# Performance work log

Hardware: AMD Instinct MI355X
Metric: run time of the kernel (lower is better)

## Reference

```python
import jax, jax.numpy as jnp
import numpy as np

B, N, D, H = 2, 1536, 1024, 16
DH = D // H
SCALE = DH ** -0.5


def setup_inputs() -> dict:
    key = jax.random.key(0)
    ks = jax.random.split(key, 16)
    s = D ** -0.5
    x = jax.random.normal(ks[0], (B, N, D), dtype=jnp.float32)
    # causal prior: 0 on/below diagonal, -1e9 above
    causal = jnp.tril(jnp.ones((N, N), dtype=bool))
    attn_bias = jnp.where(causal, 0.0, -1e9).astype(jnp.float32)[None, None]
    mk = lambda k, shp: jax.random.normal(k, shp, dtype=jnp.float32) * s
    return {
        "x": x,
        "attn_bias": attn_bias,
        "Wq": mk(ks[1], (D, D)), "bq": jnp.zeros((D,), jnp.float32),
        "Wk": mk(ks[2], (D, D)), "bk": jnp.zeros((D,), jnp.float32),
        "Wv": mk(ks[3], (D, D)), "bv": jnp.zeros((D,), jnp.float32),
        "Wg1": mk(ks[4], (D, D)), "bg1": jnp.zeros((D,), jnp.float32),
        "Wg2": mk(ks[5], (D, 1)), "bg2": jnp.zeros((1,), jnp.float32),
        "Wo": mk(ks[6], (D, D)), "bo": jnp.zeros((D,), jnp.float32),
    }


def reference(x, attn_bias, Wq, bq, Wk, bk, Wv, bv, Wg1, bg1, Wg2, bg2, Wo, bo):
    b, n, d = x.shape
    # projections -> [B, H, N, DH]
    split = lambda t: t.reshape(b, n, H, DH).swapaxes(1, 2)
    Q = split(x @ Wq + bq)
    K = split(x @ Wk + bk)
    V = split(x @ Wv + bv)
    # scores [B, H, N, N]
    attn = jnp.einsum("bhnd,bhmd->bhnm", Q, K) * SCALE + attn_bias
    attn = jax.nn.softmax(attn, axis=-1)
    # per-(batch, head, query) entropy over key axis
    entropy = -(attn * jnp.log(attn + 1e-6)).sum(-1)  # [B, H, N]
    # gate MLP (torch nn.GELU default is exact erf)
    gate = jax.nn.sigmoid(jax.nn.gelu(x @ Wg1 + bg1, approximate=False) @ Wg2 + bg2)  # [B, N, 1]
    attn = attn * gate[:, None, :, :]  # broadcast over heads, keys
    out = jnp.einsum("bhnm,bhmd->bhnd", attn, V)
    out = out.swapaxes(1, 2).reshape(b, n, d) @ Wo + bo
    return out, entropy
```

## Files before the change

kernel.cpp:

```cpp
#include <hip/hip_runtime.h>
#include <hip/hip_bf16.h>
#include <math.h>

#define Bsz  2
#define Nseq 1536
#define Dmod 1024
#define NH   16
#define DHd  64
#define MTOT (Bsz*Nseq)
#define SCALE 0.125f
#define BK   32

typedef short  short8 __attribute__((ext_vector_type(8)));
typedef float  f32x4  __attribute__((ext_vector_type(4)));
typedef unsigned short u16x4 __attribute__((ext_vector_type(4)));
typedef unsigned short ushortT;

__device__ __forceinline__ float b2f(__hip_bfloat16 v) { return __bfloat162float(v); }
__device__ __forceinline__ unsigned short f2bf(float f) {
    union { float f; unsigned u; } a; a.f = f;
    unsigned r = a.u + 0x7fffu + ((a.u >> 16) & 1u);
    return (unsigned short)(r >> 16);
}

__device__ __forceinline__ void gl2lds16(const ushortT* g, ushortT* lds) {
    __builtin_amdgcn_global_load_lds(
        (const __attribute__((address_space(1))) unsigned int*)(g),
        (__attribute__((address_space(3))) unsigned int*)(lds),
        16, 0, 0);
}

__global__ __launch_bounds__(256)
void prep_kernel(const float* W0, const float* W1, const float* W2,
                 const float* W3, const float* W4,
                 ushortT* T0, ushortT* T1, ushortT* T2, ushortT* T3, ushortT* T4,
                 const float* __restrict__ x, ushortT* __restrict__ xb,
                 float* __restrict__ glogit)
{
    const int z = blockIdx.z;
    const int t = threadIdx.x;
    if (z == 5) {
        const int bi = blockIdx.y * 16 + blockIdx.x;
        const size_t NEl = (size_t)MTOT * Dmod;
        for (size_t i = ((size_t)bi * 256 + t) * 4; i < NEl; i += (size_t)256 * 256 * 4) {
            float4 v = *(const float4*)(x + i);
            u16x4 o = { f2bf(v.x), f2bf(v.y), f2bf(v.z), f2bf(v.w) };
            *(u16x4*)(xb + i) = o;
        }
        if (t < 12) glogit[bi * 12 + t] = 0.f;
        return;
    }
    __shared__ float tile[64][65];
    const float* W = z == 0 ? W0 : z == 1 ? W1 : z == 2 ? W2 : z == 3 ? W3 : W4;
    ushortT*     T = z == 0 ? T0 : z == 1 ? T1 : z == 2 ? T2 : z == 3 ? T3 : T4;
    const int k0 = blockIdx.x * 64, n0 = blockIdx.y * 64;
    for (int i = t; i < 1024; i += 256) {
        int r = i >> 4, c4 = (i & 15) * 4;
        float4 v = *(const float4*)&W[(size_t)(k0 + r) * 1024 + n0 + c4];
        tile[r][c4 + 0] = v.x; tile[r][c4 + 1] = v.y;
        tile[r][c4 + 2] = v.z; tile[r][c4 + 3] = v.w;
    }
    __syncthreads();
    for (int i = t; i < 1024; i += 256) {
        int rn = i >> 4, ck4 = (i & 15) * 4;
        u16x4 o = { f2bf(tile[ck4 + 0][rn]), f2bf(tile[ck4 + 1][rn]),
                    f2bf(tile[ck4 + 2][rn]), f2bf(tile[ck4 + 3][rn]) };
        *(u16x4*)&T[(size_t)(n0 + rn) * 1024 + k0 + ck4] = o;
    }
}

__device__ __forceinline__
void gemm_core(const ushortT* __restrict__ A, const ushortT* __restrict__ Bt,
               int m0, int n0, ushortT* As, ushortT* Bs, f32x4 (&acc)[4][2])
{
    const int t = threadIdx.x;
    const int l = t & 63, w = t >> 6;
    const int wm = (w >> 1) * 64, wn = (w & 1) * 32;
    const int lm = l & 15, q = l >> 4;

    const int r0 = t >> 2, c0 = (t & 3) * 8;
    const ushortT* Ag0 = A  + (size_t)(m0 + r0) * 1024 + c0;
    const ushortT* Ag1 = Ag0 + (size_t)64 * 1024;
    const ushortT* Bg0 = Bt + (size_t)(n0 + r0) * 1024 + c0;
    ushortT* La0 = As + t * 8;
    ushortT* La1 = As + 2048 + t * 8;
    ushortT* Lb0 = Bs + t * 8;

    gl2lds16(Ag0, La0);
    gl2lds16(Ag1, La1);
    gl2lds16(Bg0, Lb0);

    for (int kt = 0; kt < 1024 / BK; ++kt) {
        __syncthreads();
        if (kt + 1 < 1024 / BK) {
            int ko = (kt + 1) * BK;
            int bo = ((kt + 1) & 1) ? 4096 : 0;
            int bo2 = ((kt + 1) & 1) ? 2048 : 0;
            gl2lds16(Ag0 + ko, La0 + bo);
            gl2lds16(Ag1 + ko, La1 + bo);
            gl2lds16(Bg0 + ko, Lb0 + bo2);
        }
        const ushortT* Ab = As + ((kt & 1) ? 4096 : 0);
        const ushortT* Bb = Bs + ((kt & 1) ? 2048 : 0);
        short8 af[4], bf[2];
#pragma unroll
        for (int i = 0; i < 4; ++i)
            af[i] = *(const short8*)&Ab[(wm + i * 16 + lm) * 32 + q * 8];
#pragma unroll
        for (int j = 0; j < 2; ++j)
            bf[j] = *(const short8*)&Bb[(wn + j * 16 + lm) * 32 + q * 8];
#pragma unroll
        for (int i = 0; i < 4; ++i)
#pragma unroll
            for (int j = 0; j < 2; ++j)
                acc[i][j] = __builtin_amdgcn_mfma_f32_16x16x32_bf16(af[i], bf[j], acc[i][j], 0, 0, 0);
    }
}

__device__ __forceinline__
void gemm_core_sq(const ushortT* __restrict__ A, const ushortT* __restrict__ Bt,
                  int m0, int n0, ushortT* As, ushortT* Bs, f32x4 (&acc)[2][2])
{
    const int t = threadIdx.x;
    const int l = t & 63, w = t >> 6;
    const int wm = (w >> 1) * 32, wn = (w & 1) * 32;
    const int lm = l & 15, q = l >> 4;

    const int r0 = t >> 2, c0 = (t & 3) * 8;
    const ushortT* Ag = A  + (size_t)(m0 + r0) * 1024 + c0;
    const ushortT* Bg = Bt + (size_t)(n0 + r0) * 1024 + c0;
    ushortT* La = As + t * 8;
    ushortT* Lb = Bs + t * 8;

    gl2lds16(Ag, La);
    gl2lds16(Bg, Lb);

    for (int kt = 0; kt < 1024 / BK; ++kt) {
        __syncthreads();
        if (kt + 1 < 1024 / BK) {
            int ko = (kt + 1) * BK;
            int bo = ((kt + 1) & 1) ? 2048 : 0;
            gl2lds16(Ag + ko, La + bo);
            gl2lds16(Bg + ko, Lb + bo);
        }
        const ushortT* Ab = As + ((kt & 1) ? 2048 : 0);
        const ushortT* Bb = Bs + ((kt & 1) ? 2048 : 0);
        short8 af[2], bf[2];
#pragma unroll
        for (int i = 0; i < 2; ++i) {
            af[i] = *(const short8*)&Ab[(wm + i * 16 + lm) * 32 + q * 8];
            bf[i] = *(const short8*)&Bb[(wn + i * 16 + lm) * 32 + q * 8];
        }
#pragma unroll
        for (int i = 0; i < 2; ++i)
#pragma unroll
            for (int j = 0; j < 2; ++j)
                acc[i][j] = __builtin_amdgcn_mfma_f32_16x16x32_bf16(af[i], bf[j], acc[i][j], 0, 0, 0);
    }
}

__global__ __launch_bounds__(256)
void gemm_qkvg(const ushortT* __restrict__ xb,
               const ushortT* Wt0, const ushortT* Wt1, const ushortT* Wt2, const ushortT* Wt3,
               const float* bz0, const float* bz1, const float* bz2, const float* bz3,
               const float* __restrict__ Wg2,
               ushortT* O0, ushortT* O1, ushortT* O2, float* __restrict__ glogit)
{
    __shared__ ushortT As[2 * 128 * 32];
    __shared__ ushortT Bs[2 * 64 * 32];
    const int z = blockIdx.z;
    const ushortT* Wt  = z == 0 ? Wt0 : z == 1 ? Wt1 : z == 2 ? Wt2 : Wt3;
    const float*  bias = z == 0 ? bz0 : z == 1 ? bz1 : z == 2 ? bz2 : bz3;
    const int m0 = blockIdx.y * 128, n0 = blockIdx.x * 64;

    f32x4 acc[4][2] = {};
    gemm_core(xb, Wt, m0, n0, As, Bs, acc);

    const int t = threadIdx.x, l = t & 63, w = t >> 6;
    const int wm = (w >> 1) * 64, wn = (w & 1) * 32;
    const int lm = l & 15, q = l >> 4;

    if (z == 3) {
        float part[4][4] = {};
#pragma unroll
        for (int i = 0; i < 4; ++i)
#pragma unroll
            for (int j = 0; j < 2; ++j) {
                int n = n0 + wn + j * 16 + lm;
                float bn = bias[n];
                float w2 = Wg2[n];
#pragma unroll
                for (int r = 0; r < 4; ++r) {
                    float v = acc[i][j][r] + bn;
                    v = 0.5f * v * (1.0f + erff(v * 0.70710678118654752f));
                    part[i][r] += v * w2;
                }
            }
#pragma unroll
        for (int i = 0; i < 4; ++i)
#pragma unroll
            for (int r = 0; r < 4; ++r) {
                float p = part[i][r];
#pragma unroll
                for (int msk = 1; msk < 16; msk <<= 1) p += __shfl_xor(p, msk, 16);
                if (lm == 0)
                    atomicAdd(&glogit[m0 + wm + i * 16 + q * 4 + r], p);
            }
        return;
    }

    ushortT* O = z == 0 ? O0 : z == 1 ? O1 : O2;
#pragma unroll
    for (int i = 0; i < 4; ++i)
#pragma unroll
        for (int j = 0; j < 2; ++j) {
            int n = n0 + wn + j * 16 + lm;
            float bn = bias[n];
#pragma unroll
            for (int r = 0; r < 4; ++r) {
                int m = m0 + wm + i * 16 + q * 4 + r;
                float v = acc[i][j][r] + bn;
                if (z == 0) v *= SCALE;
                if (z == 2) {
                    int b = m / Nseq, nn = m - b * Nseq;
                    int h = n >> 6, dd = n & 63;
                    O[(size_t)((b * 16 + h) * 64 + dd) * Nseq + nn] = f2bf(v);
                } else {
                    O[(size_t)m * 1024 + n] = f2bf(v);
                }
            }
        }
}

__global__ __launch_bounds__(256)
void gemm_out(const ushortT* __restrict__ AO, const ushortT* __restrict__ WtO,
              const float* __restrict__ bias, float* __restrict__ C)
{
    __shared__ ushortT As[2 * 64 * 32];
    __shared__ ushortT Bs[2 * 64 * 32];
    const int m0 = blockIdx.y * 64, n0 = blockIdx.x * 64;

    f32x4 acc[2][2] = {};
    gemm_core_sq(AO, WtO, m0, n0, As, Bs, acc);

    const int t = threadIdx.x, l = t & 63, w = t >> 6;
    const int wm = (w >> 1) * 32, wn = (w & 1) * 32;
    const int lm = l & 15, q = l >> 4;
#pragma unroll
    for (int i = 0; i < 2; ++i)
#pragma unroll
        for (int j = 0; j < 2; ++j) {
            int n = n0 + wn + j * 16 + lm;
            float bn = bias[n];
#pragma unroll
            for (int r = 0; r < 4; ++r) {
                int m = m0 + wm + i * 16 + q * 4 + r;
                C[(size_t)m * 1024 + n] = acc[i][j][r] + bn;
            }
        }
}

__global__ __launch_bounds__(128)
void attn_mfma(const ushortT* __restrict__ Q, const ushortT* __restrict__ K,
               const ushortT* __restrict__ Vt, const float* __restrict__ glogit,
               const float* __restrict__ bg2, ushortT* __restrict__ AO,
               float* __restrict__ ent)
{
    __shared__ ushortT Ps[2][32][72];
    __shared__ float mbuf[3072];

    const int t  = threadIdx.x;
    const int w  = t >> 6, l = t & 63;
    const int ln = l & 15, q4 = l >> 4;
    const int bh = blockIdx.x, b = bh >> 4, h = bh & 15;
    const int q32 = (int)gridDim.y - 1 - (int)blockIdx.y;
    const int wq = q32 * 32;
    const int kd = wq >> 6;
    const int sbmax = ((wq >> 4) & 3) + 1;

    const ushortT* Qp = Q + (size_t)(b * Nseq + wq + ln) * Dmod + h * DHd + q4 * 8;
    short8 qf[2][2];
    qf[0][0] = *(const short8*)(Qp);
    qf[0][1] = *(const short8*)(Qp + 32);
    qf[1][0] = *(const short8*)(Qp + (size_t)16 * Dmod);
    qf[1][1] = *(const short8*)(Qp + (size_t)16 * Dmod + 32);

    float l_lane[2][4] = {}, t_lane[2][4] = {};
    f32x4 oacc[2][4] = {};

    const ushortT* Kbase = K  + (size_t)(b * Nseq) * Dmod + h * DHd + q4 * 8;
    const ushortT* Vbase = Vt + ((size_t)(b * 16 + h) * 64) * Nseq + q4 * 8;

    short8 kc[4][2];
    {
        const ushortT* Kp = Kbase + (size_t)(w * 64 + ln) * Dmod;
#pragma unroll
        for (int nb = 0; nb < 4; ++nb) {
            kc[nb][0] = *(const short8*)(Kp + (size_t)nb * 16 * Dmod);
            kc[nb][1] = *(const short8*)(Kp + (size_t)nb * 16 * Dmod + 32);
        }
    }

    for (int kt = w; kt < kd; kt += 2) {
        const int k0 = kt * 64;
        const ushortT* Vp = Vbase + (size_t)ln * Nseq + k0;
        short8 vf[4][2];
#pragma unroll
        for (int nb = 0; nb < 4; ++nb) {
            vf[nb][0] = *(const short8*)(Vp + (size_t)nb * 16 * Nseq);
            vf[nb][1] = *(const short8*)(Vp + (size_t)nb * 16 * Nseq + 32);
        }
        short8 kn[4][2];
        {
            int prow = k0 + 128; if (prow > Nseq - 64) prow = Nseq - 64;
            const ushortT* Kp = Kbase + (size_t)(prow + ln) * Dmod;
#pragma unroll
            for (int nb = 0; nb < 4; ++nb) {
                kn[nb][0] = *(const short8*)(Kp + (size_t)nb * 16 * Dmod);
                kn[nb][1] = *(const short8*)(Kp + (size_t)nb * 16 * Dmod + 32);
            }
        }
        f32x4 sacc[2][4];
#pragma unroll
        for (int g = 0; g < 2; ++g)
#pragma unroll
            for (int nb = 0; nb < 4; ++nb) {
                f32x4 a = {};
                a = __builtin_amdgcn_mfma_f32_16x16x32_bf16(qf[g][0], kc[nb][0], a, 0, 0, 0);
                a = __builtin_amdgcn_mfma_f32_16x16x32_bf16(qf[g][1], kc[nb][1], a, 0, 0, 0);
                sacc[g][nb] = a;
            }
#pragma unroll
        for (int g = 0; g < 2; ++g)
#pragma unroll
            for (int nb = 0; nb < 4; ++nb)
#pragma unroll
                for (int r = 0; r < 4; ++r) {
                    float sv = sacc[g][nb][r];
                    float ev = __expf(sv);
                    l_lane[g][r] += ev;
                    t_lane[g][r] += ev * sv;
                    Ps[w][g * 16 + q4 * 4 + r][nb * 16 + ln] = f2bf(ev);
                }
        short8 pf[2][2];
#pragma unroll
        for (int g = 0; g < 2; ++g) {
            pf[g][0] = *(const short8*)&Ps[w][g * 16 + ln][q4 * 8];
            pf[g][1] = *(const short8*)&Ps[w][g * 16 + ln][32 + q4 * 8];
        }
#pragma unroll
        for (int g = 0; g < 2; ++g)
#pragma unroll
            for (int nb = 0; nb < 4; ++nb) {
                oacc[g][nb] = __builtin_amdgcn_mfma_f32_16x16x32_bf16(pf[g][0], vf[nb][0], oacc[g][nb], 0, 0, 0);
                oacc[g][nb] = __builtin_amdgcn_mfma_f32_16x16x32_bf16(pf[g][1], vf[nb][1], oacc[g][nb], 0, 0, 0);
            }
#pragma unroll
        for (int nb = 0; nb < 4; ++nb) { kc[nb][0] = kn[nb][0]; kc[nb][1] = kn[nb][1]; }
    }

    if ((kd & 1) == w) {
        const int k0 = kd * 64;
        const ushortT* Vp = Vbase + (size_t)ln * Nseq + k0;
        short8 vf[4][2];
#pragma unroll
        for (int nb = 0; nb < 4; ++nb) {
            vf[nb][0] = *(const short8*)(Vp + (size_t)nb * 16 * Nseq);
            vf[nb][1] = *(const short8*)(Vp + (size_t)nb * 16 * Nseq + 32);
        }
        f32x4 sacc[2][4];
#pragma unroll
        for (int g = 0; g < 2; ++g)
#pragma unroll
            for (int nb = 0; nb < 4; ++nb)
                if (nb <= sbmax) {
                    f32x4 a = {};
                    a = __builtin_amdgcn_mfma_f32_16x16x32_bf16(qf[g][0], kc[nb][0], a, 0, 0, 0);
                    a = __builtin_amdgcn_mfma_f32_16x16x32_bf16(qf[g][1], kc[nb][1], a, 0, 0, 0);
                    sacc[g][nb] = a;
                }
#pragma unroll
        for (int g = 0; g < 2; ++g)
#pragma unroll
            for (int nb = 0; nb < 4; ++nb)
#pragma unroll
                for (int r = 0; r < 4; ++r) {
                    float ev = 0.f;
                    if (nb <= sbmax) {
                        int kg = k0 + nb * 16 + ln;
                        int qg = wq + g * 16 + q4 * 4 + r;
                        float sv = sacc[g][nb][r];
                        ev = (kg <= qg) ? __expf(sv) : 0.f;
                        l_lane[g][r] += ev;
                        t_lane[g][r] += ev * sv;
                    }
                    Ps[w][g * 16 + q4 * 4 + r][nb * 16 + ln] = f2bf(ev);
                }
        short8 pf[2][2];
#pragma unroll
        for (int g = 0; g < 2; ++g) {
            pf[g][0] = *(const short8*)&Ps[w][g * 16 + ln][q4 * 8];
            pf[g][1] = *(const short8*)&Ps[w][g * 16 + ln][32 + q4 * 8];
        }
#pragma unroll
        for (int g = 0; g < 2; ++g)
#pragma unroll
            for (int nb = 0; nb < 4; ++nb) {
                oacc[g][nb] = __builtin_amdgcn_mfma_f32_16x16x32_bf16(pf[g][0], vf[nb][0], oacc[g][nb], 0, 0, 0);
                oacc[g][nb] = __builtin_amdgcn_mfma_f32_16x16x32_bf16(pf[g][1], vf[nb][1], oacc[g][nb], 0, 0, 0);
            }
    }

    if (w == 1) {
#pragma unroll
        for (int g = 0; g < 2; ++g)
#pragma unroll
            for (int nb = 0; nb < 4; ++nb)
#pragma unroll
                for (int r = 0; r < 4; ++r)
                    mbuf[(((g << 2) | nb) * 4 + r) * 64 + l] = oacc[g][nb][r];
#pragma unroll
        for (int g = 0; g < 2; ++g)
#pragma unroll
            for (int r = 0; r < 4; ++r) {
                mbuf[2048 + ((g << 2) | r) * 64 + l] = l_lane[g][r];
                mbuf[2560 + ((g << 2) | r) * 64 + l] = t_lane[g][r];
            }
    }
    __syncthreads();
    if (w == 1) return;
#pragma unroll
    for (int g = 0; g < 2; ++g) {
#pragma unroll
        for (int nb = 0; nb < 4; ++nb)
#pragma unroll
            for (int r = 0; r < 4; ++r)
                oacc[g][nb][r] += mbuf[(((g << 2) | nb) * 4 + r) * 64 + l];
#pragma unroll
        for (int r = 0; r < 4; ++r) {
            l_lane[g][r] += mbuf[2048 + ((g << 2) | r) * 64 + l];
            t_lane[g][r] += mbuf[2560 + ((g << 2) | r) * 64 + l];
        }
    }

    const float bg2v = bg2[0];
#pragma unroll
    for (int g = 0; g < 2; ++g) {
        float sc[4];
#pragma unroll
        for (int r = 0; r < 4; ++r) {
            float lv = l_lane[g][r], tv = t_lane[g][r];
#pragma unroll
            for (int msk = 1; msk < 16; msk <<= 1) {
                lv += __shfl_xor(lv, msk, 16);
                tv += __shfl_xor(tv, msk, 16);
            }
            int qg = wq + g * 16 + q4 * 4 + r;
            float inv = 1.f / lv;
            if (ln == 0)
                ent[((size_t)b * NH + h) * Nseq + qg] = logf(lv) - tv * inv;
            float logit = glogit[b * Nseq + qg] + bg2v;
            sc[r] = inv / (1.f + __expf(-logit));
        }
#pragma unroll
        for (int nb = 0; nb < 4; ++nb)
#pragma unroll
            for (int r = 0; r < 4; ++r) {
                int qg = wq + g * 16 + q4 * 4 + r;
                AO[(size_t)(b * Nseq + qg) * Dmod + h * DHd + nb * 16 + ln] =
                    f2bf(oacc[g][nb][r] * sc[r]);
            }
    }
}

extern "C" void kernel_launch(void* const* d_in, const int* in_sizes, int n_in,
                              void* d_out, int out_size, void* d_ws, size_t ws_size,
                              hipStream_t stream)
{
    const float* x   = (const float*)d_in[0];
    const float* Wq  = (const float*)d_in[2];
    const float* bq  = (const float*)d_in[3];
    const float* Wk  = (const float*)d_in[4];
    const float* bk  = (const float*)d_in[5];
    const float* Wv  = (const float*)d_in[6];
    const float* bv  = (const float*)d_in[7];
    const float* Wg1 = (const float*)d_in[8];
    const float* bg1 = (const float*)d_in[9];
    const float* Wg2 = (const float*)d_in[10];
    const float* bg2 = (const float*)d_in[11];
    const float* Wo  = (const float*)d_in[12];
    const float* bo  = (const float*)d_in[13];

    const size_t NE = (size_t)MTOT * Dmod;
    ushortT* p   = (ushortT*)d_ws;
    ushortT* Qw  = p; p += NE;
    ushortT* Kw  = p; p += NE;
    ushortT* Vtw = p; p += NE;
    ushortT* AO  = p; p += NE;
    ushortT* xb  = p; p += NE;
    ushortT* WtQ = p; p += (size_t)1024 * 1024;
    ushortT* WtK = p; p += (size_t)1024 * 1024;
    ushortT* WtV = p; p += (size_t)1024 * 1024;
    ushortT* WtG = p; p += (size_t)1024 * 1024;
    ushortT* WtO = p; p += (size_t)1024 * 1024;
    float* glogit = (float*)p;

    float* out_f = (float*)d_out;
    float* ent_f = out_f + NE;

    prep_kernel<<<dim3(16, 16, 6), 256, 0, stream>>>(Wq, Wk, Wv, Wg1, Wo,
                                                     WtQ, WtK, WtV, WtG, WtO,
                                                     x, xb, glogit);
    gemm_qkvg<<<dim3(16, 24, 4), 256, 0, stream>>>(xb, WtQ, WtK, WtV, WtG,
                                                   bq, bk, bv, bg1, Wg2,
                                                   Qw, Kw, Vtw, glogit);
    attn_mfma<<<dim3(Bsz * NH, Nseq / 32), 128, 0, stream>>>(Qw, Kw, Vtw, glogit,
                                                             bg2, AO, ent_f);
    gemm_out<<<dim3(16, 48), 256, 0, stream>>>(AO, WtO, bo, out_f);
}
```

Measured before the change: 231.0 us.

## Rewrite QKV+gate projection GEMM as 256x256-tile 8-wave pipelined kernel

Replaces the 128x64-tile, 4-wave projection GEMM with a 256x256-tile, 512-thread kernel that treats the four weight matrices as one contiguous 4096-wide matrix. It uses BK=64, XOR-swizzled LDS staging, and quarter-staged prefetching interleaved with MFMA phases under explicit waitcnt/barrier/setprio control. Block IDs are remapped for L2 locality. The goal is more data reuse per LDS load and less per-block overhead, at the cost of high register pressure, only 192 blocks, and the implicit assumption that WtQ..WtG are contiguous in memory.

After: 269.1 us. 1.17x slower.

```diff
diff --git a/kernel.cpp b/kernel.cpp
--- a/kernel.cpp
+++ b/kernel.cpp
@@ -69,52 +69,184 @@
     }
 }
 
-__device__ __forceinline__
-void gemm_core(const ushortT* __restrict__ A, const ushortT* __restrict__ Bt,
-               int m0, int n0, ushortT* As, ushortT* Bs, f32x4 (&acc)[4][2])
+#define MFMA16(a, b, c) __builtin_amdgcn_mfma_f32_16x16x32_bf16((a), (b), (c), 0, 0, 0)
+
+__global__ __launch_bounds__(512, 2)
+void gemm_qkvg(const ushortT* __restrict__ xb, const ushortT* __restrict__ Wt,
+               const float* __restrict__ bz0, const float* __restrict__ bz1,
+               const float* __restrict__ bz2, const float* __restrict__ bz3,
+               const float* __restrict__ Wg2,
+               ushortT* __restrict__ O0, ushortT* __restrict__ O1,
+               ushortT* __restrict__ O2, float* __restrict__ glogit)
 {
+    __shared__ ushortT As[2][256 * 64];
+    __shared__ ushortT Bs[2][256 * 64];
+
+    const int bid = blockIdx.y * 16 + blockIdx.x;
+    const int wg  = (bid & 7) * 24 + (bid >> 3);
+    const int bx = wg & 15, by = wg >> 4;
+    const int m0 = by * 256, n0 = bx * 256;
+
     const int t = threadIdx.x;
     const int l = t & 63, w = t >> 6;
-    const int wm = (w >> 1) * 64, wn = (w & 1) * 32;
-    const int lm = l & 15, q = l >> 4;
-
-    const int r0 = t >> 2, c0 = (t & 3) * 8;
-    const ushortT* Ag0 = A  + (size_t)(m0 + r0) * 1024 + c0;
-    const ushortT* Ag1 = Ag0 + (size_t)64 * 1024;
-    const ushortT* Bg0 = Bt + (size_t)(n0 + r0) * 1024 + c0;
-    ushortT* La0 = As + t * 8;
-    ushortT* La1 = As + 2048 + t * 8;
-    ushortT* Lb0 = Bs + t * 8;
-
-    gl2lds16(Ag0, La0);
-    gl2lds16(Ag1, La1);
-    gl2lds16(Bg0, Lb0);
-
-    for (int kt = 0; kt < 1024 / BK; ++kt) {
-        __syncthreads();
-        if (kt + 1 < 1024 / BK) {
-            int ko = (kt + 1) * BK;
-            int bo = ((kt + 1) & 1) ? 4096 : 0;
-            int bo2 = ((kt + 1) & 1) ? 2048 : 0;
-            gl2lds16(Ag0 + ko, La0 + bo);
-            gl2lds16(Ag1 + ko, La1 + bo);
-            gl2lds16(Bg0 + ko, Lb0 + bo2);
-        }
-        const ushortT* Ab = As + ((kt & 1) ? 4096 : 0);
-        const ushortT* Bb = Bs + ((kt & 1) ? 2048 : 0);
-        short8 af[4], bf[2];
-#pragma unroll
-        for (int i = 0; i < 4; ++i)
-            af[i] = *(const short8*)&Ab[(wm + i * 16 + lm) * 32 + q * 8];
-#pragma unroll
-        for (int j = 0; j < 2; ++j)
-            bf[j] = *(const short8*)&Bb[(wn + j * 16 + lm) * 32 + q * 8];
-#pragma unroll
-        for (int i = 0; i < 4; ++i)
-#pragma unroll
-            for (int j = 0; j < 2; ++j)
-                acc[i][j] = __builtin_amdgcn_mfma_f32_16x16x32_bf16(af[i], bf[j], acc[i][j], 0, 0, 0);
-    }
+    const int wr = w >> 2, wc = w & 3;
+    const int lm = l & 15, q4 = l >> 4;
+
+    const int tr = t >> 3;
+    const int sg = ((t & 7) ^ (tr & 7)) * 8;
+    const ushortT* Asrc = xb + (size_t)(m0 + tr) * 1024 + sg;
+    const ushortT* Bsrc = Wt + (size_t)(n0 + tr) * 1024 + sg;
+
+#define STG_A(buf, s, k_) gl2lds16(Asrc + (size_t)(s) * 64 * 1024 + (k_), &As[buf][(s) * 4096 + t * 8])
+#define STG_B(buf, s, k_) gl2lds16(Bsrc + (size_t)(s) * 64 * 1024 + (k_), &Bs[buf][(s) * 4096 + t * 8])
+
+    const int slot0 = (q4 ^ (lm & 7)) * 8;
+    const int aOff  = (wr * 16 + lm) * 64;
+    const int bOff  = (wc * 16 + lm) * 64;
+
+#define RDA(buf, f, kk) (*(const short8*)&As[buf][aOff + (f) * 2048 + (slot0 ^ ((kk) * 32))])
+#define RDB(buf, j, kk) (*(const short8*)&Bs[buf][bOff + (j) * 4096 + (slot0 ^ ((kk) * 32))])
+
+    f32x4 acc[8][4] = {};
+    short8 afr[4][2], bfr[4][2];
+
+    STG_A(0, 0, 0); STG_A(0, 1, 0);
+    STG_B(0, 0, 0); STG_B(0, 1, 0);
+    STG_B(0, 2, 0); STG_B(0, 3, 0);
+    STG_A(0, 2, 0); STG_A(0, 3, 0);
+    asm volatile("s_waitcnt vmcnt(4)" ::: "memory");
+    __builtin_amdgcn_s_barrier();
+
+    for (int kt = 0; kt < 16; ++kt) {
+        const int cur = kt & 1, nxt = cur ^ 1;
+        const int kN = (kt + 1) * 64;
+        const bool more = (kt < 15);
+
+#pragma unroll
+        for (int f = 0; f < 4; ++f) { afr[f][0] = RDA(cur, f, 0); afr[f][1] = RDA(cur, f, 1); }
+#pragma unroll
+        for (int j = 0; j < 2; ++j) { bfr[j][0] = RDB(cur, j, 0); bfr[j][1] = RDB(cur, j, 1); }
+        if (more) { STG_A(nxt, 0, kN); STG_A(nxt, 1, kN); }
+        __builtin_amdgcn_s_barrier();
+        asm volatile("s_waitcnt lgkmcnt(0)" ::: "memory");
+        __builtin_amdgcn_sched_barrier(0);
+        __builtin_amdgcn_s_setprio(1);
+#pragma unroll
+        for (int f = 0; f < 4; ++f)
+#pragma unroll
+            for (int j = 0; j < 2; ++j) {
+                acc[f][j] = MFMA16(afr[f][0], bfr[j][0], acc[f][j]);
+                acc[f][j] = MFMA16(afr[f][1], bfr[j][1], acc[f][j]);
+            }
+        __builtin_amdgcn_s_setprio(0);
+        __builtin_amdgcn_sched_barrier(0);
+        if (more) asm volatile("s_waitcnt vmcnt(4)" ::: "memory");
+        else      asm volatile("s_waitcnt vmcnt(2)" ::: "memory");
+        __builtin_amdgcn_s_barrier();
+
+#pragma unroll
+        for (int j = 2; j < 4; ++j) { bfr[j][0] = RDB(cur, j, 0); bfr[j][1] = RDB(cur, j, 1); }
+        if (more) { STG_B(nxt, 0, kN); STG_B(nxt, 1, kN); }
+        __builtin_amdgcn_s_barrier();
+        asm volatile("s_waitcnt lgkmcnt(0)" ::: "memory");
+        __builtin_amdgcn_sched_barrier(0);
+        __builtin_amdgcn_s_setprio(1);
+#pragma unroll
+        for (int f = 0; f < 4; ++f)
+#pragma unroll
+            for (int j = 2; j < 4; ++j) {
+                acc[f][j] = MFMA16(afr[f][0], bfr[j][0], acc[f][j]);
+                acc[f][j] = MFMA16(afr[f][1], bfr[j][1], acc[f][j]);
+            }
+        __builtin_amdgcn_s_setprio(0);
+        __builtin_amdgcn_sched_barrier(0);
+        if (more) asm volatile("s_waitcnt vmcnt(4)" ::: "memory");
+        else      asm volatile("s_waitcnt vmcnt(0)" ::: "memory");
+        __builtin_amdgcn_s_barrier();
+
+#pragma unroll
+        for (int f = 0; f < 4; ++f) { afr[f][0] = RDA(cur, f + 4, 0); afr[f][1] = RDA(cur, f + 4, 1); }
+        if (more) { STG_B(nxt, 2, kN); STG_B(nxt, 3, kN); }
+        __builtin_amdgcn_s_barrier();
+        asm volatile("s_waitcnt lgkmcnt(0)" ::: "memory");
+        __builtin_amdgcn_sched_barrier(0);
+        __builtin_amdgcn_s_setprio(1);
+#pragma unroll
+        for (int f = 0; f < 4; ++f)
+#pragma unroll
+            for (int j = 2; j < 4; ++j) {
+                acc[f + 4][j] = MFMA16(afr[f][0], bfr[j][0], acc[f + 4][j]);
+                acc[f + 4][j] = MFMA16(afr[f][1], bfr[j][1], acc[f + 4][j]);
+            }
+        __builtin_amdgcn_s_setprio(0);
+        __builtin_amdgcn_s_barrier();
+
+        if (more) { STG_A(nxt, 2, kN); STG_A(nxt, 3, kN); }
+        __builtin_amdgcn_s_barrier();
+        __builtin_amdgcn_s_setprio(1);
+#pragma unroll
+        for (int f = 0; f < 4; ++f)
+#pragma unroll
+            for (int j = 0; j < 2; ++j) {
+                acc[f + 4][j] = MFMA16(afr[f][0], bfr[j][0], acc[f + 4][j]);
+                acc[f + 4][j] = MFMA16(afr[f][1], bfr[j][1], acc[f + 4][j]);
+            }
+        __builtin_amdgcn_s_setprio(0);
+        __builtin_amdgcn_sched_barrier(0);
+        if (more) asm volatile("s_waitcnt vmcnt(4)" ::: "memory");
+        __builtin_amdgcn_s_barrier();
+    }
+
+    const int z = bx >> 2;
+    if (z == 3) {
+        float part[8][4] = {};
+#pragma unroll
+        for (int f = 0; f < 8; ++f)
+#pragma unroll
+            for (int j = 0; j < 4; ++j) {
+                int nn = (n0 & 1023) + j * 64 + wc * 16 + lm;
+                float bn = bz3[nn], w2 = Wg2[nn];
+#pragma unroll
+                for (int r = 0; r < 4; ++r) {
+                    float v = acc[f][j][r] + bn;
+                    v = 0.5f * v * (1.0f + erff(v * 0.70710678118654752f));
+                    part[f][r] += v * w2;
+                }
+            }
+#pragma unroll
+        for (int f = 0; f < 8; ++f)
+#pragma unroll
+            for (int r = 0; r < 4; ++r) {
+                float p = part[f][r];
+#pragma unroll
+                for (int msk = 1; msk < 16; msk <<= 1) p += __shfl_xor(p, msk, 16);
+                if (lm == 0)
+                    atomicAdd(&glogit[m0 + f * 32 + wr * 16 + q4 * 4 + r], p);
+            }
+        return;
+    }
+    const float* bias = z == 0 ? bz0 : z == 1 ? bz1 : bz2;
+    ushortT* O = z == 0 ? O0 : z == 1 ? O1 : O2;
+#pragma unroll
+    for (int f = 0; f < 8; ++f)
+#pragma unroll
+        for (int j = 0; j < 4; ++j) {
+            int nn = (n0 & 1023) + j * 64 + wc * 16 + lm;
+            float bn = bias[nn];
+#pragma unroll
+            for (int r = 0; r < 4; ++r) {
+                int m = m0 + f * 32 + wr * 16 + q4 * 4 + r;
+                float v = acc[f][j][r] + bn;
+                if (z == 0) v *= SCALE;
+                if (z == 2) {
+                    int bb = m >= Nseq ? 1 : 0, nn2 = m - bb * Nseq;
+                    int h = nn >> 6, dd = nn & 63;
+                    O[(size_t)((bb * 16 + h) * 64 + dd) * Nseq + nn2] = f2bf(v);
+                } else {
+                    O[(size_t)m * 1024 + nn] = f2bf(v);
+                }
+            }
+        }
 }
 
 __device__ __forceinline__
@@ -157,79 +289,6 @@
             for (int j = 0; j < 2; ++j)
                 acc[i][j] = __builtin_amdgcn_mfma_f32_16x16x32_bf16(af[i], bf[j], acc[i][j], 0, 0, 0);
     }
-}
-
-__global__ __launch_bounds__(256)
-void gemm_qkvg(const ushortT* __restrict__ xb,
-               const ushortT* Wt0, const ushortT* Wt1, const ushortT* Wt2, const ushortT* Wt3,
-               const float* bz0, const float* bz1, const float* bz2, const float* bz3,
-               const float* __restrict__ Wg2,
-               ushortT* O0, ushortT* O1, ushortT* O2, float* __restrict__ glogit)
-{
-    __shared__ ushortT As[2 * 128 * 32];
-    __shared__ ushortT Bs[2 * 64 * 32];
-    const int z = blockIdx.z;
-    const ushortT* Wt  = z == 0 ? Wt0 : z == 1 ? Wt1 : z == 2 ? Wt2 : Wt3;
-    const float*  bias = z == 0 ? bz0 : z == 1 ? bz1 : z == 2 ? bz2 : bz3;
-    const int m0 = blockIdx.y * 128, n0 = blockIdx.x * 64;
-
-    f32x4 acc[4][2] = {};
-    gemm_core(xb, Wt, m0, n0, As, Bs, acc);
-
-    const int t = threadIdx.x, l = t & 63, w = t >> 6;
-    const int wm = (w >> 1) * 64, wn = (w & 1) * 32;
-    const int lm = l & 15, q = l >> 4;
-
-    if (z == 3) {
-        float part[4][4] = {};
-#pragma unroll
-        for (int i = 0; i < 4; ++i)
-#pragma unroll
-            for (int j = 0; j < 2; ++j) {
-                int n = n0 + wn + j * 16 + lm;
-                float bn = bias[n];
-                float w2 = Wg2[n];
-#pragma unroll
-                for (int r = 0; r < 4; ++r) {
-                    float v = acc[i][j][r] + bn;
-                    v = 0.5f * v * (1.0f + erff(v * 0.70710678118654752f));
-                    part[i][r] += v * w2;
-                }
-            }
-#pragma unroll
-        for (int i = 0; i < 4; ++i)
-#pragma unroll
-            for (int r = 0; r < 4; ++r) {
-                float p = part[i][r];
-#pragma unroll
-                for (int msk = 1; msk < 16; msk <<= 1) p += __shfl_xor(p, msk, 16);
-                if (lm == 0)
-                    atomicAdd(&glogit[m0 + wm + i * 16 + q * 4 + r], p);
-            }
-        return;
-    }
-
-    ushortT* O = z == 0 ? O0 : z == 1 ? O1 : O2;
-#pragma unroll
-    for (int i = 0; i < 4; ++i)
-#pragma unroll
-        for (int j = 0; j < 2; ++j) {
-            int n = n0 + wn + j * 16 + lm;
-            float bn = bias[n];
-#pragma unroll
-            for (int r = 0; r < 4; ++r) {
-                int m = m0 + wm + i * 16 + q * 4 + r;
-                float v = acc[i][j][r] + bn;
-                if (z == 0) v *= SCALE;
-                if (z == 2) {
-                    int b = m / Nseq, nn = m - b * Nseq;
-                    int h = n >> 6, dd = n & 63;
-                    O[(size_t)((b * 16 + h) * 64 + dd) * Nseq + nn] = f2bf(v);
-                } else {
-                    O[(size_t)m * 1024 + n] = f2bf(v);
-                }
-            }
-        }
 }
 
 __global__ __launch_bounds__(256)
@@ -511,9 +570,9 @@
     prep_kernel<<<dim3(16, 16, 6), 256, 0, stream>>>(Wq, Wk, Wv, Wg1, Wo,
                                                      WtQ, WtK, WtV, WtG, WtO,
                                                      x, xb, glogit);
-    gemm_qkvg<<<dim3(16, 24, 4), 256, 0, stream>>>(xb, WtQ, WtK, WtV, WtG,
-                                                   bq, bk, bv, bg1, Wg2,
-                                                   Qw, Kw, Vtw, glogit);
+    gemm_qkvg<<<dim3(16, 12), 512, 0, stream>>>(xb, WtQ,
+                                                bq, bk, bv, bg1, Wg2,
+                                                Qw, Kw, Vtw, glogit);
     attn_mfma<<<dim3(Bsz * NH, Nseq / 32), 128, 0, stream>>>(Qw, Kw, Vtw, glogit,
                                                              bg2, AO, ent_f);
     gemm_out<<<dim3(16, 48), 256, 0, stream>>>(AO, WtO, bo, out_f);
```

## Compute transposed scores so P stays in registers, dropping the LDS round-trip

Applied to the files above, without the earlier changes.

The attention kernel now computes S^T by swapping the MFMA operands. Each lane then holds four consecutive keys for one query, and those exps can be packed straight into bf16 A-operands, using v_cvt_pk_bf16_f32, for 16x16x16 MFMAs against V. This removes the per-tile write of P to shared memory and the read back, and it shrinks the row-sum and entropy accumulators and their cross-lane reductions. The trade is twice as many, smaller MFMAs and narrower 8-byte V loads, and the row sums have to be reshuffled for the output scale.

New measurement: 244.5 us. 5.8% more time.

```diff
diff --git a/kernel.cpp b/kernel.cpp
--- a/kernel.cpp
+++ b/kernel.cpp
@@ -12,6 +12,7 @@
 #define BK   32
 
 typedef short  short8 __attribute__((ext_vector_type(8)));
+typedef short  s16x4  __attribute__((ext_vector_type(4)));
 typedef float  f32x4  __attribute__((ext_vector_type(4)));
 typedef unsigned short u16x4 __attribute__((ext_vector_type(4)));
 typedef unsigned short ushortT;
@@ -23,12 +24,21 @@
     return (unsigned short)(r >> 16);
 }
 
+__device__ __forceinline__ unsigned cvtpk2(float a, float b) {
+    unsigned r;
+    asm("v_cvt_pk_bf16_f32 %0, %1, %2" : "=v"(r) : "v"(a), "v"(b));
+    return r;
+}
+
 __device__ __forceinline__ void gl2lds16(const ushortT* g, ushortT* lds) {
     __builtin_amdgcn_global_load_lds(
         (const __attribute__((address_space(1))) unsigned int*)(g),
         (__attribute__((address_space(3))) unsigned int*)(lds),
         16, 0, 0);
 }
+
+#define MFMA16(a, b, c) __builtin_amdgcn_mfma_f32_16x16x32_bf16((a), (b), (c), 0, 0, 0)
+#define MFMA16K(a, b, c) __builtin_amdgcn_mfma_f32_16x16x16bf16_1k((a), (b), (c), 0, 0, 0)
 
 __global__ __launch_bounds__(256)
 void prep_kernel(const float* W0, const float* W1, const float* W2,
@@ -117,48 +127,6 @@
     }
 }
 
-__device__ __forceinline__
-void gemm_core_sq(const ushortT* __restrict__ A, const ushortT* __restrict__ Bt,
-                  int m0, int n0, ushortT* As, ushortT* Bs, f32x4 (&acc)[2][2])
-{
-    const int t = threadIdx.x;
-    const int l = t & 63, w = t >> 6;
-    const int wm = (w >> 1) * 32, wn = (w & 1) * 32;
-    const int lm = l & 15, q = l >> 4;
-
-    const int r0 = t >> 2, c0 = (t & 3) * 8;
-    const ushortT* Ag = A  + (size_t)(m0 + r0) * 1024 + c0;
-    const ushortT* Bg = Bt + (size_t)(n0 + r0) * 1024 + c0;
-    ushortT* La = As + t * 8;
-    ushortT* Lb = Bs + t * 8;
-
-    gl2lds16(Ag, La);
-    gl2lds16(Bg, Lb);
-
-    for (int kt = 0; kt < 1024 / BK; ++kt) {
-        __syncthreads();
-        if (kt + 1 < 1024 / BK) {
-            int ko = (kt + 1) * BK;
-            int bo = ((kt + 1) & 1) ? 2048 : 0;
-            gl2lds16(Ag + ko, La + bo);
-            gl2lds16(Bg + ko, Lb + bo);
-        }
-        const ushortT* Ab = As + ((kt & 1) ? 2048 : 0);
-        const ushortT* Bb = Bs + ((kt & 1) ? 2048 : 0);
-        short8 af[2], bf[2];
-#pragma unroll
-        for (int i = 0; i < 2; ++i) {
-            af[i] = *(const short8*)&Ab[(wm + i * 16 + lm) * 32 + q * 8];
-            bf[i] = *(const short8*)&Bb[(wn + i * 16 + lm) * 32 + q * 8];
-        }
-#pragma unroll
-        for (int i = 0; i < 2; ++i)
-#pragma unroll
-            for (int j = 0; j < 2; ++j)
-                acc[i][j] = __builtin_amdgcn_mfma_f32_16x16x32_bf16(af[i], bf[j], acc[i][j], 0, 0, 0);
-    }
-}
-
 __global__ __launch_bounds__(256)
 void gemm_qkvg(const ushortT* __restrict__ xb,
                const ushortT* Wt0, const ushortT* Wt1, const ushortT* Wt2, const ushortT* Wt3,
@@ -178,7 +146,7 @@
 
     const int t = threadIdx.x, l = t & 63, w = t >> 6;
     const int wm = (w >> 1) * 64, wn = (w & 1) * 32;
-    const int lm = l & 15, q = l >> 4;
+    const int lm = l & 15, q4 = l >> 4;
 
     if (z == 3) {
         float part[4][4] = {};
@@ -204,7 +172,7 @@
 #pragma unroll
                 for (int msk = 1; msk < 16; msk <<= 1) p += __shfl_xor(p, msk, 16);
                 if (lm == 0)
-                    atomicAdd(&glogit[m0 + wm + i * 16 + q * 4 + r], p);
+                    atomicAdd(&glogit[m0 + wm + i * 16 + q4 * 4 + r], p);
             }
         return;
     }
@@ -218,7 +186,7 @@
             float bn = bias[n];
 #pragma unroll
             for (int r = 0; r < 4; ++r) {
-                int m = m0 + wm + i * 16 + q * 4 + r;
+                int m = m0 + wm + i * 16 + q4 * 4 + r;
                 float v = acc[i][j][r] + bn;
                 if (z == 0) v *= SCALE;
                 if (z == 2) {
@@ -232,6 +200,48 @@
         }
 }
 
+__device__ __forceinline__
+void gemm_core_sq(const ushortT* __restrict__ A, const ushortT* __restrict__ Bt,
+                  int m0, int n0, ushortT* As, ushortT* Bs, f32x4 (&acc)[2][2])
+{
+    const int t = threadIdx.x;
+    const int l = t & 63, w = t >> 6;
+    const int wm = (w >> 1) * 32, wn = (w & 1) * 32;
+    const int lm = l & 15, q = l >> 4;
+
+    const int r0 = t >> 2, c0 = (t & 3) * 8;
+    const ushortT* Ag = A  + (size_t)(m0 + r0) * 1024 + c0;
+    const ushortT* Bg = Bt + (size_t)(n0 + r0) * 1024 + c0;
+    ushortT* La = As + t * 8;
+    ushortT* Lb = Bs + t * 8;
+
+    gl2lds16(Ag, La);
+    gl2lds16(Bg, Lb);
+
+    for (int kt = 0; kt < 1024 / BK; ++kt) {
+        __syncthreads();
+        if (kt + 1 < 1024 / BK) {
+            int ko = (kt + 1) * BK;
+            int bo = ((kt + 1) & 1) ? 2048 : 0;
+            gl2lds16(Ag + ko, La + bo);
+            gl2lds16(Bg + ko, Lb + bo);
+        }
+        const ushortT* Ab = As + ((kt & 1) ? 2048 : 0);
+        const ushortT* Bb = Bs + ((kt & 1) ? 2048 : 0);
+        short8 af[2], bf[2];
+#pragma unroll
+        for (int i = 0; i < 2; ++i) {
+            af[i] = *(const short8*)&Ab[(wm + i * 16 + lm) * 32 + q * 8];
+            bf[i] = *(const short8*)&Bb[(wn + i * 16 + lm) * 32 + q * 8];
+        }
+#pragma unroll
+        for (int i = 0; i < 2; ++i)
+#pragma unroll
+            for (int j = 0; j < 2; ++j)
+                acc[i][j] = __builtin_amdgcn_mfma_f32_16x16x32_bf16(af[i], bf[j], acc[i][j], 0, 0, 0);
+    }
+}
+
 __global__ __launch_bounds__(256)
 void gemm_out(const ushortT* __restrict__ AO, const ushortT* __restrict__ WtO,
               const float* __restrict__ bias, float* __restrict__ C)
@@ -266,8 +276,7 @@
                const float* __restrict__ bg2, ushortT* __restrict__ AO,
                float* __restrict__ ent)
 {
-    __shared__ ushortT Ps[2][32][72];
-    __shared__ float mbuf[3072];
+    __shared__ float mbuf[2304];
 
     const int t  = threadIdx.x;
     const int w  = t >> 6, l = t & 63;
@@ -285,11 +294,12 @@
     qf[1][0] = *(const short8*)(Qp + (size_t)16 * Dmod);
     qf[1][1] = *(const short8*)(Qp + (size_t)16 * Dmod + 32);
 
-    float l_lane[2][4] = {}, t_lane[2][4] = {};
+    float l_lane[2] = {}, t_lane[2] = {};
     f32x4 oacc[2][4] = {};
 
     const ushortT* Kbase = K  + (size_t)(b * Nseq) * Dmod + h * DHd + q4 * 8;
-    const ushortT* Vbase = Vt + ((size_t)(b * 16 + h) * 64) * Nseq + q4 * 8;
+    const ushortT* Vlane = Vt + (size_t)(b * 16 + h) * 64 * Nseq
+                              + (size_t)ln * Nseq + q4 * 4;
 
     short8 kc[4][2];
     {
@@ -303,13 +313,12 @@
 
     for (int kt = w; kt < kd; kt += 2) {
         const int k0 = kt * 64;
-        const ushortT* Vp = Vbase + (size_t)ln * Nseq + k0;
-        short8 vf[4][2];
-#pragma unroll
-        for (int nb = 0; nb < 4; ++nb) {
-            vf[nb][0] = *(const short8*)(Vp + (size_t)nb * 16 * Nseq);
-            vf[nb][1] = *(const short8*)(Vp + (size_t)nb * 16 * Nseq + 32);
-        }
+        s16x4 vf[4][4];
+#pragma unroll
+        for (int ks = 0; ks < 4; ++ks)
+#pragma unroll
+            for (int db = 0; db < 4; ++db)
+                vf[ks][db] = *(const s16x4*)(Vlane + (size_t)db * 16 * Nseq + k0 + ks * 16);
         short8 kn[4][2];
         {
             int prow = k0 + 128; if (prow > Nseq - 64) prow = Nseq - 64;
@@ -326,48 +335,44 @@
 #pragma unroll
             for (int nb = 0; nb < 4; ++nb) {
                 f32x4 a = {};
-                a = __builtin_amdgcn_mfma_f32_16x16x32_bf16(qf[g][0], kc[nb][0], a, 0, 0, 0);
-                a = __builtin_amdgcn_mfma_f32_16x16x32_bf16(qf[g][1], kc[nb][1], a, 0, 0, 0);
+                a = MFMA16(kc[nb][0], qf[g][0], a);
+                a = MFMA16(kc[nb][1], qf[g][1], a);
                 sacc[g][nb] = a;
             }
-#pragma unroll
-        for (int g = 0; g < 2; ++g)
-#pragma unroll
-            for (int nb = 0; nb < 4; ++nb)
-#pragma unroll
-                for (int r = 0; r < 4; ++r) {
-                    float sv = sacc[g][nb][r];
-                    float ev = __expf(sv);
-                    l_lane[g][r] += ev;
-                    t_lane[g][r] += ev * sv;
-                    Ps[w][g * 16 + q4 * 4 + r][nb * 16 + ln] = f2bf(ev);
-                }
-        short8 pf[2][2];
-#pragma unroll
-        for (int g = 0; g < 2; ++g) {
-            pf[g][0] = *(const short8*)&Ps[w][g * 16 + ln][q4 * 8];
-            pf[g][1] = *(const short8*)&Ps[w][g * 16 + ln][32 + q4 * 8];
-        }
+        s16x4 pa[2][4];
 #pragma unroll
         for (int g = 0; g < 2; ++g)
 #pragma unroll
             for (int nb = 0; nb < 4; ++nb) {
-                oacc[g][nb] = __builtin_amdgcn_mfma_f32_16x16x32_bf16(pf[g][0], vf[nb][0], oacc[g][nb], 0, 0, 0);
-                oacc[g][nb] = __builtin_amdgcn_mfma_f32_16x16x32_bf16(pf[g][1], vf[nb][1], oacc[g][nb], 0, 0, 0);
-            }
+                f32x4 s4 = sacc[g][nb];
+                float e0 = __expf(s4[0]), e1 = __expf(s4[1]);
+                float e2 = __expf(s4[2]), e3 = __expf(s4[3]);
+                l_lane[g] += (e0 + e1) + (e2 + e3);
+                t_lane[g] += (e0 * s4[0] + e1 * s4[1]) + (e2 * s4[2] + e3 * s4[3]);
+                union { unsigned u[2]; s16x4 v; } pk_;
+                pk_.u[0] = cvtpk2(e0, e1);
+                pk_.u[1] = cvtpk2(e2, e3);
+                pa[g][nb] = pk_.v;
+            }
+#pragma unroll
+        for (int g = 0; g < 2; ++g)
+#pragma unroll
+            for (int db = 0; db < 4; ++db)
+#pragma unroll
+                for (int ks = 0; ks < 4; ++ks)
+                    oacc[g][db] = MFMA16K(pa[g][ks], vf[ks][db], oacc[g][db]);
 #pragma unroll
         for (int nb = 0; nb < 4; ++nb) { kc[nb][0] = kn[nb][0]; kc[nb][1] = kn[nb][1]; }
     }
 
     if ((kd & 1) == w) {
         const int k0 = kd * 64;
-        const ushortT* Vp = Vbase + (size_t)ln * Nseq + k0;
-        short8 vf[4][2];
-#pragma unroll
-        for (int nb = 0; nb < 4; ++nb) {
-            vf[nb][0] = *(const short8*)(Vp + (size_t)nb * 16 * Nseq);
-            vf[nb][1] = *(const short8*)(Vp + (size_t)nb * 16 * Nseq + 32);
-        }
+        s16x4 vf[4][4];
+#pragma unroll
+        for (int ks = 0; ks < 4; ++ks)
+#pragma unroll
+            for (int db = 0; db < 4; ++db)
+                vf[ks][db] = *(const s16x4*)(Vlane + (size_t)db * 16 * Nseq + k0 + ks * 16);
         f32x4 sacc[2][4];
 #pragma unroll
         for (int g = 0; g < 2; ++g)
@@ -375,40 +380,40 @@
             for (int nb = 0; nb < 4; ++nb)
                 if (nb <= sbmax) {
                     f32x4 a = {};
-                    a = __builtin_amdgcn_mfma_f32_16x16x32_bf16(qf[g][0], kc[nb][0], a, 0, 0, 0);
-                    a = __builtin_amdgcn_mfma_f32_16x16x32_bf16(qf[g][1], kc[nb][1], a, 0, 0, 0);
+                    a = MFMA16(kc[nb][0], qf[g][0], a);
+                    a = MFMA16(kc[nb][1], qf[g][1], a);
                     sacc[g][nb] = a;
                 }
-#pragma unroll
-        for (int g = 0; g < 2; ++g)
-#pragma unroll
-            for (int nb = 0; nb < 4; ++nb)
-#pragma unroll
-                for (int r = 0; r < 4; ++r) {
-                    float ev = 0.f;
-                    if (nb <= sbmax) {
-                        int kg = k0 + nb * 16 + ln;
-                        int qg = wq + g * 16 + q4 * 4 + r;
-                        float sv = sacc[g][nb][r];
-                        ev = (kg <= qg) ? __expf(sv) : 0.f;
-                        l_lane[g][r] += ev;
-                        t_lane[g][r] += ev * sv;
-                    }
-                    Ps[w][g * 16 + q4 * 4 + r][nb * 16 + ln] = f2bf(ev);
+        s16x4 pa[2][4];
+#pragma unroll
+        for (int g = 0; g < 2; ++g)
+#pragma unroll
+            for (int nb = 0; nb < 4; ++nb) {
+                union { unsigned u[2]; s16x4 v; } pk_;
+                if (nb <= sbmax) {
+                    f32x4 s4 = sacc[g][nb];
+                    int qg = wq + g * 16 + ln;
+                    int kb = k0 + nb * 16 + q4 * 4;
+                    float e0 = (kb + 0 <= qg) ? __expf(s4[0]) : 0.f;
+                    float e1 = (kb + 1 <= qg) ? __expf(s4[1]) : 0.f;
+                    float e2 = (kb + 2 <= qg) ? __expf(s4[2]) : 0.f;
+                    float e3 = (kb + 3 <= qg) ? __expf(s4[3]) : 0.f;
+                    l_lane[g] += (e0 + e1) + (e2 + e3);
+                    t_lane[g] += (e0 * s4[0] + e1 * s4[1]) + (e2 * s4[2] + e3 * s4[3]);
+                    pk_.u[0] = cvtpk2(e0, e1);
+                    pk_.u[1] = cvtpk2(e2, e3);
+                } else {
+                    pk_.u[0] = 0; pk_.u[1] = 0;
                 }
-        short8 pf[2][2];
-#pragma unroll
-        for (int g = 0; g < 2; ++g) {
-            pf[g][0] = *(const short8*)&Ps[w][g * 16 + ln][q4 * 8];
-            pf[g][1] = *(const short8*)&Ps[w][g * 16 + ln][32 + q4 * 8];
-        }
-#pragma unroll
-        for (int g = 0; g < 2; ++g)
-#pragma unroll
-            for (int nb = 0; nb < 4; ++nb) {
-                oacc[g][nb] = __builtin_amdgcn_mfma_f32_16x16x32_bf16(pf[g][0], vf[nb][0], oacc[g][nb], 0, 0, 0);
-                oacc[g][nb] = __builtin_amdgcn_mfma_f32_16x16x32_bf16(pf[g][1], vf[nb][1], oacc[g][nb], 0, 0, 0);
-            }
+                pa[g][nb] = pk_.v;
+            }
+#pragma unroll
+        for (int g = 0; g < 2; ++g)
+#pragma unroll
+            for (int db = 0; db < 4; ++db)
+#pragma unroll
+                for (int ks = 0; ks < 4; ++ks)
+                    oacc[g][db] = MFMA16K(pa[g][ks], vf[ks][db], oacc[g][db]);
     }
 
     if (w == 1) {
@@ -420,12 +425,10 @@
                 for (int r = 0; r < 4; ++r)
                     mbuf[(((g << 2) | nb) * 4 + r) * 64 + l] = oacc[g][nb][r];
 #pragma unroll
-        for (int g = 0; g < 2; ++g)
-#pragma unroll
-            for (int r = 0; r < 4; ++r) {
-                mbuf[2048 + ((g << 2) | r) * 64 + l] = l_lane[g][r];
-                mbuf[2560 + ((g << 2) | r) * 64 + l] = t_lane[g][r];
-            }
+        for (int g = 0; g < 2; ++g) {
+            mbuf[2048 + g * 64 + l] = l_lane[g];
+            mbuf[2176 + g * 64 + l] = t_lane[g];
+        }
     }
     __syncthreads();
     if (w == 1) return;
@@ -436,31 +439,25 @@
 #pragma unroll
             for (int r = 0; r < 4; ++r)
                 oacc[g][nb][r] += mbuf[(((g << 2) | nb) * 4 + r) * 64 + l];
+        l_lane[g] += mbuf[2048 + g * 64 + l];
+        t_lane[g] += mbuf[2176 + g * 64 + l];
+    }
+
+    const float bg2v = bg2[0];
+#pragma unroll
+    for (int g = 0; g < 2; ++g) {
+        float lv = l_lane[g], tv = t_lane[g];
+        lv += __shfl_xor(lv, 16); lv += __shfl_xor(lv, 32);
+        tv += __shfl_xor(tv, 16); tv += __shfl_xor(tv, 32);
+        if (q4 == 0)
+            ent[((size_t)b * NH + h) * Nseq + wq + g * 16 + ln] = logf(lv) - tv / lv;
+        float sc[4];
 #pragma unroll
         for (int r = 0; r < 4; ++r) {
-            l_lane[g][r] += mbuf[2048 + ((g << 2) | r) * 64 + l];
-            t_lane[g][r] += mbuf[2560 + ((g << 2) | r) * 64 + l];
-        }
-    }
-
-    const float bg2v = bg2[0];
-#pragma unroll
-    for (int g = 0; g < 2; ++g) {
-        float sc[4];
-#pragma unroll
-        for (int r = 0; r < 4; ++r) {
-            float lv = l_lane[g][r], tv = t_lane[g][r];
-#pragma unroll
-            for (int msk = 1; msk < 16; msk <<= 1) {
-                lv += __shfl_xor(lv, msk, 16);
-                tv += __shfl_xor(tv, msk, 16);
-            }
-            int qg = wq + g * 16 + q4 * 4 + r;
-            float inv = 1.f / lv;
-            if (ln == 0)
-                ent[((size_t)b * NH + h) * Nseq + qg] = logf(lv) - tv * inv;
-            float logit = glogit[b * Nseq + qg] + bg2v;
-            sc[r] = inv / (1.f + __expf(-logit));
+            int rr = q4 * 4 + r;
+            float lrr = __shfl(lv, (l & 48) + rr);
+            float logit = glogit[b * Nseq + wq + g * 16 + rr] + bg2v;
+            sc[r] = (1.f / lrr) / (1.f + __expf(-logit));
         }
 #pragma unroll
         for (int nb = 0; nb < 4; ++nb)
```
